# Optimization experiments

Measured on AMD Instinct MI355X. Metric: run time of the kernel, lower is better.

## Reference

```python
import jax, jax.numpy as jnp
import numpy as np

N_NODES = 17   # fixed by Linear(256, 17) + residual add
D = 512        # feature dim
H = 8          # number of attention heads


def setup_inputs() -> dict:
    key = jax.random.key(0)
    ks = jax.random.split(key, 8)
    return {
        "Xs": jax.random.normal(ks[0], (N_NODES, D), dtype=jnp.float32),
        "ROIs_b": jax.random.uniform(ks[1], (N_NODES, 3), dtype=jnp.float32),
        "adj": jnp.zeros((N_NODES, N_NODES), dtype=jnp.float32),  # unused in forward
        "FC": jax.random.normal(ks[2], (H, D, D), dtype=jnp.float32) * (1.414 / np.sqrt(D)),
        "W1": jax.random.normal(ks[3], (H, D + 3, 256), dtype=jnp.float32) * (1.0 / np.sqrt(D + 3)),
        "b1": jnp.zeros((H, 256), dtype=jnp.float32),
        "W2": jax.random.normal(ks[4], (H, 256, N_NODES), dtype=jnp.float32) * (1.0 / np.sqrt(256)),
        "b2": jnp.zeros((H, N_NODES), dtype=jnp.float32),
        "conv_w": jax.random.normal(ks[5], (H,), dtype=jnp.float32) * 0.3,
        "conv_b": jnp.zeros((1,), dtype=jnp.float32),
    }


def reference(Xs, ROIs_b, adj, FC, W1, b1, W2, b2, conv_w, conv_b):
    # All 8 heads batched over leading axis h (original launches them as
    # separate Python-level modules).
    # f_input = relu(Xs @ FC) per head: [H, N, D]
    f = jax.nn.relu(jnp.einsum('nd,hde->hne', Xs, FC))
    # concat coordinates: [H, N, D+3]
    coords = jnp.broadcast_to(ROIs_b[None], (f.shape[0], ROIs_b.shape[0], ROIs_b.shape[1]))
    cat = jnp.concatenate([f, coords], axis=-1)
    # 2-layer MLP: Linear(515,256) -> tanh -> Linear(256,17): [H, N, 17]
    hdn = jnp.tanh(jnp.einsum('hnc,hcm->hnm', cat, W1) + b1[:, None, :])
    att = jnp.einsum('hnm,hmk->hnk', hdn, W2) + b2[:, None, :]
    # permute(1,0) then softmax over dim=1 (the N axis): [H, 17, N]
    att = jax.nn.softmax(jnp.swapaxes(att, 1, 2), axis=-1)
    # weighted sum over nodes: [H, 17, D]
    h_prime = jnp.einsum('hkn,hnd->hkd', att, f)
    # Conv1d(8,1,1) over head axis + ReLU, then residual
    out = jax.nn.relu(jnp.einsum('h,hkd->kd', conv_w, h_prime) + conv_b[0])
    Xs_out = out + Xs  # [17, 512]
    # original returns a list of per-landmark views [1,512,1,1,1]; we return
    # the equivalent stacked array plus passthrough ROIs
    return Xs_out, ROIs_b
```

## Files before the change

kernel.cpp:

```cpp
#include <hip/hip_runtime.h>

#define NN 17
#define D  512
#define H  8
#define C1 515
#define M  256

#define NBLOCKS 128

#define XPAD 20
#define RSN  36
#define RSG  (NN * RSN)
#define SMEM_FL (32 * RSG)

__device__ __forceinline__ void fma4(float4& a, float x, const float4& w) {
    a.x = fmaf(x, w.x, a.x); a.y = fmaf(x, w.y, a.y);
    a.z = fmaf(x, w.z, a.z); a.w = fmaf(x, w.w, a.w);
}

__device__ __forceinline__ void store_agent(float* p, float v) {
    __hip_atomic_store(p, v, __ATOMIC_RELAXED, __HIP_MEMORY_SCOPE_AGENT);
}

__device__ __forceinline__ void grid_barrier(unsigned int* ctr, unsigned int nb) {
    asm volatile("s_waitcnt vmcnt(0)" ::: "memory");
    __syncthreads();
    if (threadIdx.x == 0) {
        __hip_atomic_fetch_add(ctr, 1u, __ATOMIC_RELAXED, __HIP_MEMORY_SCOPE_AGENT);
        while (__hip_atomic_load(ctr, __ATOMIC_RELAXED, __HIP_MEMORY_SCOPE_AGENT) < nb) {
            __builtin_amdgcn_s_sleep(2);
        }
    }
    __syncthreads();
}

__global__ __launch_bounds__(256) void fused_all(
        const float* __restrict__ Xs,     const float* __restrict__ ROIs,
        const float* __restrict__ FC,     const float* __restrict__ W1,
        const float* __restrict__ b1,     const float* __restrict__ W2,
        const float* __restrict__ b2,     const float* __restrict__ conv_w,
        const float* __restrict__ conv_b, float* __restrict__ out,
        float* __restrict__ f,            float* __restrict__ hdn,
        unsigned int* __restrict__ ctrs) {
    const int b = blockIdx.x;
    const int t = threadIdx.x;
    __shared__ __align__(16) float sm[SMEM_FL];

    {
        const int et = b & 15, h = b >> 4;
        const int tw = t & 7, cgr = t >> 3;
        for (int i = t; i < NN * D; i += 256) {
            const int n = i >> 9, d = i & 511;
            sm[d * XPAD + n] = Xs[i];
        }
        __syncthreads();
        float4 acc[NN];
#pragma unroll
        for (int n = 0; n < NN; ++n) acc[n] = make_float4(0.f, 0.f, 0.f, 0.f);
        const float4* fc4 = (const float4*)(FC + (size_t)h * D * D) + et * 8 + tw;
#pragma unroll 4
        for (int i = 0; i < 16; ++i) {
            const int d = cgr + (i << 5);
            const float4 w = fc4[d << 7];
            const float* xr = sm + d * XPAD;
#pragma unroll
            for (int n4 = 0; n4 < 4; ++n4) {
                const float4 x = *(const float4*)(xr + (n4 << 2));
                fma4(acc[n4 * 4 + 0], x.x, w);
                fma4(acc[n4 * 4 + 1], x.y, w);
                fma4(acc[n4 * 4 + 2], x.z, w);
                fma4(acc[n4 * 4 + 3], x.w, w);
            }
            fma4(acc[16], xr[16], w);
        }
        __syncthreads();
        float* rr = sm + cgr * RSG + tw * 4;
#pragma unroll
        for (int n = 0; n < NN; ++n) *(float4*)(rr + n * RSN) = acc[n];
        __syncthreads();
        for (int i = t; i < NN * 32; i += 256) {
            const int n = i >> 5, e = i & 31;
            float s = 0.f;
#pragma unroll 8
            for (int g = 0; g < 32; ++g) s += sm[g * RSG + n * RSN + e];
            store_agent(&f[((h * NN + n) << 9) + (et << 5) + e], fmaxf(s, 0.f));
        }
    }
    grid_barrier(ctrs + 0, NBLOCKS);

    if (b < H * 8) {
        const int mt = b & 7, h = b >> 3;
        const int tw = t & 7, cgr = t >> 3;
        for (int i = t; i < NN * D; i += 256) {
            const int n = i >> 9, d = i & 511;
            sm[d * XPAD + n] = f[((size_t)(h * NN) << 9) + i];
        }
        if (t < NN * 3) {
            const int n = t / 3, cc = t % 3;
            sm[(D + cc) * XPAD + n] = ROIs[t];
        }
        __syncthreads();
        float4 acc[NN];
#pragma unroll
        for (int n = 0; n < NN; ++n) acc[n] = make_float4(0.f, 0.f, 0.f, 0.f);
        const float4* w4 = (const float4*)(W1 + (size_t)h * C1 * M) + mt * 8 + tw;
#pragma unroll 4
        for (int i = 0; i < 16; ++i) {
            const int c = cgr + (i << 5);
            const float4 w = w4[c << 6];
            const float* xr = sm + c * XPAD;
#pragma unroll
            for (int n4 = 0; n4 < 4; ++n4) {
                const float4 x = *(const float4*)(xr + (n4 << 2));
                fma4(acc[n4 * 4 + 0], x.x, w);
                fma4(acc[n4 * 4 + 1], x.y, w);
                fma4(acc[n4 * 4 + 2], x.z, w);
                fma4(acc[n4 * 4 + 3], x.w, w);
            }
            fma4(acc[16], xr[16], w);
        }
        if (cgr < 3) {
            const int c = D + cgr;
            const float4 w = w4[c << 6];
            const float* xr = sm + c * XPAD;
#pragma unroll
            for (int n4 = 0; n4 < 4; ++n4) {
                const float4 x = *(const float4*)(xr + (n4 << 2));
                fma4(acc[n4 * 4 + 0], x.x, w);
                fma4(acc[n4 * 4 + 1], x.y, w);
                fma4(acc[n4 * 4 + 2], x.z, w);
                fma4(acc[n4 * 4 + 3], x.w, w);
            }
            fma4(acc[16], xr[16], w);
        }
        __syncthreads();
        float* rr = sm + cgr * RSG + tw * 4;
#pragma unroll
        for (int n = 0; n < NN; ++n) *(float4*)(rr + n * RSN) = acc[n];
        __syncthreads();
        for (int i = t; i < NN * 32; i += 256) {
            const int n = i >> 5, m = i & 31;
            float s = b1[h * M + (mt << 5) + m];
#pragma unroll 8
            for (int g = 0; g < 32; ++g) s += sm[g * RSG + n * RSN + m];
            store_agent(&hdn[(h * NN + n) * M + (mt << 5) + m], tanhf(s));
        }
    }
    grid_barrier(ctrs + 32, NBLOCKS);

    if (b < NN) {
        const int k = b;
        float* swk = sm;
        float* sa  = sm + H * (M + 4);
        float* cwv = sm + H * (M + 4) + H * NN;
        for (int i = t; i < H * M; i += 256) {
            const int h = i >> 8, m = i & 255;
            swk[h * (M + 4) + m] = W2[(size_t)(h * M + m) * NN + k];
        }
        if (t < H) cwv[t] = conv_w[t];
        __syncthreads();
        if (t < H * NN) {
            const int h = t / NN, n = t % NN;
            const float4* a4 = (const float4*)(hdn + (h * NN + n) * M);
            const float4* w4 = (const float4*)(swk + h * (M + 4));
            float acc = b2[h * NN + k];
#pragma unroll 8
            for (int m4 = 0; m4 < M / 4; ++m4) {
                const float4 av = a4[m4];
                const float4 wv = w4[m4];
                acc = fmaf(av.x, wv.x, acc); acc = fmaf(av.y, wv.y, acc);
                acc = fmaf(av.z, wv.z, acc); acc = fmaf(av.w, wv.w, acc);
            }
            sa[h * NN + n] = acc;
        }
        __syncthreads();
        if (t < H) {
            float mx = -1e30f;
#pragma unroll
            for (int n = 0; n < NN; ++n) mx = fmaxf(mx, sa[t * NN + n]);
            float e[NN];
            float s = 0.f;
#pragma unroll
            for (int n = 0; n < NN; ++n) { e[n] = __expf(sa[t * NN + n] - mx); s += e[n]; }
            const float inv = 1.f / s;
#pragma unroll
            for (int n = 0; n < NN; ++n) sa[t * NN + n] = e[n] * inv;
        }
        __syncthreads();
        const float cb = conv_b[0];
        float acc0 = 0.f, acc1 = 0.f;
        for (int h = 0; h < H; ++h) {
            float w0 = 0.f, w1 = 0.f;
#pragma unroll
            for (int n = 0; n < NN; ++n) {
                const float a = sa[h * NN + n];
                const float* fr = f + (size_t)((h * NN + n) << 9);
                w0 = fmaf(a, fr[t], w0);
                w1 = fmaf(a, fr[t + 256], w1);
            }
            acc0 = fmaf(cwv[h], w0, acc0);
            acc1 = fmaf(cwv[h], w1, acc1);
        }
        out[(k << 9) + t]       = fmaxf(acc0 + cb, 0.f) + Xs[(k << 9) + t];
        out[(k << 9) + t + 256] = fmaxf(acc1 + cb, 0.f) + Xs[(k << 9) + t + 256];
        if (k == 0 && t < NN * 3) out[NN * D + t] = ROIs[t];
    }
}

extern "C" void kernel_launch(void* const* d_in, const int* in_sizes, int n_in,
                              void* d_out, int out_size, void* d_ws, size_t ws_size,
                              hipStream_t stream) {
    const float* Xs     = (const float*)d_in[0];
    const float* ROIs   = (const float*)d_in[1];
    const float* FC     = (const float*)d_in[3];
    const float* W1     = (const float*)d_in[4];
    const float* b1     = (const float*)d_in[5];
    const float* W2     = (const float*)d_in[6];
    const float* b2     = (const float*)d_in[7];
    const float* conv_w = (const float*)d_in[8];
    const float* conv_b = (const float*)d_in[9];
    float* outp = (float*)d_out;

    float* fbuf   = (float*)d_ws;
    float* hdnbuf = fbuf + H * NN * D;

    unsigned int* ctrs = (unsigned int*)((char*)d_ws + (1u << 20));
    hipMemsetAsync(ctrs, 0, 256, stream);

    fused_all<<<NBLOCKS, 256, 0, stream>>>(Xs, ROIs, FC, W1, b1, W2, b2,
                                           conv_w, conv_b, outp, fbuf, hdnbuf,
                                           ctrs);
}
```

Baseline: 114.8 us.

## Replace grid barriers with per-head counters and prefetch weights before waits

Swaps the two full-grid barriers for finer-grained dependency counters: stage 2 blocks wait only for the 16 stage-1 blocks of their own head, and stage 3 waits on a counter that each head bumps once all of its 8 hidden tiles are done. Blocks that have no later work exit early. FC and W1 weight tiles are loaded into registers ahead of the waits so global latency overlaps the synchronisation. This raises register pressure (about 17 float4 values of weights plus 17 accumulators) and depends on the relaxed atomics together with s_waitcnt for correct ordering.

```diff
diff --git a/kernel.cpp b/kernel.cpp
--- a/kernel.cpp
+++ b/kernel.cpp
@@ -13,6 +13,10 @@
 #define RSG  (NN * RSN)
 #define SMEM_FL (32 * RSG)
 
+#define CTR1(h)  ((h) * 32)
+#define CTR2H(h) (256 + (h) * 32)
+#define CTR2F    512
+
 __device__ __forceinline__ void fma4(float4& a, float x, const float4& w) {
     a.x = fmaf(x, w.x, a.x); a.y = fmaf(x, w.y, a.y);
     a.z = fmaf(x, w.z, a.z); a.w = fmaf(x, w.w, a.w);
@@ -22,13 +26,20 @@
     __hip_atomic_store(p, v, __ATOMIC_RELAXED, __HIP_MEMORY_SCOPE_AGENT);
 }
 
-__device__ __forceinline__ void grid_barrier(unsigned int* ctr, unsigned int nb) {
+__device__ __forceinline__ unsigned ctr_add(unsigned* c) {
+    return __hip_atomic_fetch_add(c, 1u, __ATOMIC_RELAXED, __HIP_MEMORY_SCOPE_AGENT);
+}
+
+__device__ __forceinline__ void arrive(unsigned* c) {
     asm volatile("s_waitcnt vmcnt(0)" ::: "memory");
     __syncthreads();
+    if (threadIdx.x == 0) ctr_add(c);
+}
+
+__device__ __forceinline__ void wait_ge(unsigned* c, unsigned nb) {
     if (threadIdx.x == 0) {
-        __hip_atomic_fetch_add(ctr, 1u, __ATOMIC_RELAXED, __HIP_MEMORY_SCOPE_AGENT);
-        while (__hip_atomic_load(ctr, __ATOMIC_RELAXED, __HIP_MEMORY_SCOPE_AGENT) < nb) {
-            __builtin_amdgcn_s_sleep(2);
+        while (__hip_atomic_load(c, __ATOMIC_RELAXED, __HIP_MEMORY_SCOPE_AGENT) < nb) {
+            __builtin_amdgcn_s_sleep(1);
         }
     }
     __syncthreads();
@@ -44,11 +55,15 @@
         unsigned int* __restrict__ ctrs) {
     const int b = blockIdx.x;
     const int t = threadIdx.x;
+    const int tw = t & 7, cgr = t >> 3;
     __shared__ __align__(16) float sm[SMEM_FL];
 
     {
-        const int et = b & 15, h = b >> 4;
-        const int tw = t & 7, cgr = t >> 3;
+        const int et = b & 15, h1 = b >> 4;
+        float4 wreg[16];
+        const float4* fc4 = (const float4*)(FC + (size_t)h1 * D * D) + et * 8 + tw;
+#pragma unroll
+        for (int i = 0; i < 16; ++i) wreg[i] = fc4[(cgr + (i << 5)) << 7];
         for (int i = t; i < NN * D; i += 256) {
             const int n = i >> 9, d = i & 511;
             sm[d * XPAD + n] = Xs[i];
@@ -57,12 +72,10 @@
         float4 acc[NN];
 #pragma unroll
         for (int n = 0; n < NN; ++n) acc[n] = make_float4(0.f, 0.f, 0.f, 0.f);
-        const float4* fc4 = (const float4*)(FC + (size_t)h * D * D) + et * 8 + tw;
-#pragma unroll 4
+#pragma unroll
         for (int i = 0; i < 16; ++i) {
-            const int d = cgr + (i << 5);
-            const float4 w = fc4[d << 7];
-            const float* xr = sm + d * XPAD;
+            const float4 w = wreg[i];
+            const float* xr = sm + (cgr + (i << 5)) * XPAD;
 #pragma unroll
             for (int n4 = 0; n4 < 4; ++n4) {
                 const float4 x = *(const float4*)(xr + (n4 << 2));
@@ -83,17 +96,24 @@
             float s = 0.f;
 #pragma unroll 8
             for (int g = 0; g < 32; ++g) s += sm[g * RSG + n * RSN + e];
-            store_agent(&f[((h * NN + n) << 9) + (et << 5) + e], fmaxf(s, 0.f));
-        }
-    }
-    grid_barrier(ctrs + 0, NBLOCKS);
-
-    if (b < H * 8) {
-        const int mt = b & 7, h = b >> 3;
-        const int tw = t & 7, cgr = t >> 3;
+            store_agent(&f[((h1 * NN + n) << 9) + (et << 5) + e], fmaxf(s, 0.f));
+        }
+        arrive(ctrs + CTR1(h1));
+    }
+    if (b >= H * 8) return;
+
+    {
+        const int mt = b & 7, h2 = b >> 3;
+        float4 w1r[17];
+        const float4* w4 = (const float4*)(W1 + (size_t)h2 * C1 * M) + mt * 8 + tw;
+#pragma unroll
+        for (int i = 0; i < 16; ++i) w1r[i] = w4[(cgr + (i << 5)) << 6];
+        w1r[16] = (cgr < 3) ? w4[(D + cgr) << 6] : make_float4(0.f, 0.f, 0.f, 0.f);
+        __builtin_amdgcn_sched_barrier(0);
+        wait_ge(ctrs + CTR1(h2), 16);
         for (int i = t; i < NN * D; i += 256) {
             const int n = i >> 9, d = i & 511;
-            sm[d * XPAD + n] = f[((size_t)(h * NN) << 9) + i];
+            sm[d * XPAD + n] = f[((size_t)(h2 * NN) << 9) + i];
         }
         if (t < NN * 3) {
             const int n = t / 3, cc = t % 3;
@@ -103,12 +123,10 @@
         float4 acc[NN];
 #pragma unroll
         for (int n = 0; n < NN; ++n) acc[n] = make_float4(0.f, 0.f, 0.f, 0.f);
-        const float4* w4 = (const float4*)(W1 + (size_t)h * C1 * M) + mt * 8 + tw;
-#pragma unroll 4
+#pragma unroll
         for (int i = 0; i < 16; ++i) {
-            const int c = cgr + (i << 5);
-            const float4 w = w4[c << 6];
-            const float* xr = sm + c * XPAD;
+            const float4 w = w1r[i];
+            const float* xr = sm + (cgr + (i << 5)) * XPAD;
 #pragma unroll
             for (int n4 = 0; n4 < 4; ++n4) {
                 const float4 x = *(const float4*)(xr + (n4 << 2));
@@ -120,9 +138,8 @@
             fma4(acc[16], xr[16], w);
         }
         if (cgr < 3) {
-            const int c = D + cgr;
-            const float4 w = w4[c << 6];
-            const float* xr = sm + c * XPAD;
+            const float4 w = w1r[16];
+            const float* xr = sm + (D + cgr) * XPAD;
 #pragma unroll
             for (int n4 = 0; n4 < 4; ++n4) {
                 const float4 x = *(const float4*)(xr + (n4 << 2));
@@ -140,15 +157,20 @@
         __syncthreads();
         for (int i = t; i < NN * 32; i += 256) {
             const int n = i >> 5, m = i & 31;
-            float s = b1[h * M + (mt << 5) + m];
+            float s = b1[h2 * M + (mt << 5) + m];
 #pragma unroll 8
             for (int g = 0; g < 32; ++g) s += sm[g * RSG + n * RSN + m];
-            store_agent(&hdn[(h * NN + n) * M + (mt << 5) + m], tanhf(s));
-        }
-    }
-    grid_barrier(ctrs + 32, NBLOCKS);
-
-    if (b < NN) {
+            store_agent(&hdn[(h2 * NN + n) * M + (mt << 5) + m], tanhf(s));
+        }
+        asm volatile("s_waitcnt vmcnt(0)" ::: "memory");
+        __syncthreads();
+        if (t == 0) {
+            if (ctr_add(ctrs + CTR2H(h2)) == 7u) ctr_add(ctrs + CTR2F);
+        }
+    }
+    if (b >= NN) return;
+
+    {
         const int k = b;
         float* swk = sm;
         float* sa  = sm + H * (M + 4);
@@ -158,7 +180,8 @@
             swk[h * (M + 4) + m] = W2[(size_t)(h * M + m) * NN + k];
         }
         if (t < H) cwv[t] = conv_w[t];
-        __syncthreads();
+        __builtin_amdgcn_sched_barrier(0);
+        wait_ge(ctrs + CTR2F, 8);
         if (t < H * NN) {
             const int h = t / NN, n = t % NN;
             const float4* a4 = (const float4*)(hdn + (h * NN + n) * M);
@@ -225,7 +248,7 @@
     float* hdnbuf = fbuf + H * NN * D;
 
     unsigned int* ctrs = (unsigned int*)((char*)d_ws + (1u << 20));
-    hipMemsetAsync(ctrs, 0, 256, stream);
+    hipMemsetAsync(ctrs, 0, (512 + 32) * sizeof(unsigned int), stream);
 
     fused_all<<<NBLOCKS, 256, 0, stream>>>(Xs, ROIs, FC, W1, b1, W2, b2,
                                            conv_w, conv_b, outp, fbuf, hdnbuf,
```

Result: faster. 108.6 us (-5.4%).
